# Kernel optimization log

Hardware: AMD Instinct MI355X
Metric: run time of the kernel (lower is better)

The kernel has to match this reference:

```python
import jax, jax.numpy as jnp
import numpy as np

N_NODES = 100000
N_EDGES = 1600000
D_FEAT = 64


def setup_inputs() -> dict:
    key = jax.random.key(0)
    k1, k2, k3, k4 = jax.random.split(key, 4)
    x = jax.random.normal(k1, (N_NODES, D_FEAT), dtype=jnp.float32)
    edge_values = jax.random.uniform(k2, (N_EDGES,), dtype=jnp.float32)
    # row-sorted targets mimic a coalesced sparse COO matrix
    target_index = jnp.sort(jax.random.randint(k3, (N_EDGES,), 0, N_NODES, dtype=jnp.int32))
    source_index = jax.random.randint(k4, (N_EDGES,), 0, N_NODES, dtype=jnp.int32)
    return {"x": x, "edge_values": edge_values,
            "target_index": target_index, "source_index": source_index}


def reference(x, edge_values, target_index, source_index):
    # sparsify_message: gather source rows -> [n_edges, d]
    msg = x[source_index]
    # scale by sparse neighborhood values
    msg = edge_values[:, None] * msg
    # aggregate: scatter-sum into target cells -> [n_nodes, d]
    out = jax.ops.segment_sum(msg, target_index, num_segments=N_NODES)
    return out
```

## Files before the change

### kernel.cpp

```cpp
#include <hip/hip_runtime.h>
#include <hip/hip_fp16.h>

#define N_NODES 100000
#define N_EDGES 1600000
#define D_FEAT 64

typedef __attribute__((ext_vector_type(4))) _Float16 half4v;

__global__ __launch_bounds__(256) void prep_kernel(
    const float4* __restrict__ x4,
    const int*    __restrict__ tgt,
    half4v*       __restrict__ xh,
    int*          __restrict__ row_ptr,
    int conv_blocks)
{
    const int bid = blockIdx.x;
    if (bid < conv_blocks) {
        int i = bid * 256 + threadIdx.x;
        if (i < N_NODES * 16) {
            float4 v = x4[i];
            half4v h;
            h.x = (_Float16)v.x; h.y = (_Float16)v.y;
            h.z = (_Float16)v.z; h.w = (_Float16)v.w;
            xh[i] = h;
        }
    } else {
        int e = (bid - conv_blocks) * 256 + threadIdx.x;
        if (e >= N_EDGES) return;
        int cur = tgt[e];
        int lo  = (e == 0) ? 0 : tgt[e - 1] + 1;
        for (int n = lo; n <= cur; ++n) row_ptr[n] = e;
        if (e == N_EDGES - 1) {
            for (int n = cur + 1; n <= N_NODES; ++n) row_ptr[n] = N_EDGES;
        }
    }
}

__global__ __launch_bounds__(256) void build_row_ptr(
    const int* __restrict__ tgt, int* __restrict__ row_ptr)
{
    int e = blockIdx.x * blockDim.x + threadIdx.x;
    if (e >= N_EDGES) return;
    int cur = tgt[e];
    int lo  = (e == 0) ? 0 : tgt[e - 1] + 1;
    for (int n = lo; n <= cur; ++n) row_ptr[n] = e;
    if (e == N_EDGES - 1) {
        for (int n = cur + 1; n <= N_NODES; ++n) row_ptr[n] = N_EDGES;
    }
}

#define GROUPS_PER_BLOCK 16
#define LDS_STRIDE_B     144

__global__ __launch_bounds__(256) void gather_sum_h(
    const half4v* __restrict__ xh,
    const float*  __restrict__ ev,
    const int*    __restrict__ src,
    const int*    __restrict__ row_ptr,
    float4*       __restrict__ out4)
{
    __shared__ char lds_raw[GROUPS_PER_BLOCK * LDS_STRIDE_B];

    const int tib  = threadIdx.x;
    const int gib  = tib >> 4;
    const int lane = tib & 15;
    const int node = blockIdx.x * GROUPS_PER_BLOCK + gib;
    if (node >= N_NODES) return;

    char* gbase = lds_raw + gib * LDS_STRIDE_B;

    const int start = row_ptr[node];
    const int end   = row_ptr[node + 1];

    float4 acc = make_float4(0.f, 0.f, 0.f, 0.f);

    for (int blk = start; blk < end; blk += 16) {
        const int bcnt = end - blk;

        int   s_ = 0; float w_ = 0.0f;
        if (lane < bcnt) { s_ = src[blk + lane]; w_ = ev[blk + lane]; }
        ((int2*)gbase)[lane] = make_int2(s_, __float_as_int(w_));

        const int nch = (min(bcnt, 16) + 3) >> 2;

        int4 m01 = ((const int4*)gbase)[0];
        int4 m23 = ((const int4*)gbase)[1];
        half4v x0 = xh[m01.x * 16 + lane];
        half4v x1 = xh[m01.z * 16 + lane];
        half4v x2 = xh[m23.x * 16 + lane];
        half4v x3 = xh[m23.z * 16 + lane];
        float w0 = __int_as_float(m01.y), w1 = __int_as_float(m01.w);
        float w2 = __int_as_float(m23.y), w3 = __int_as_float(m23.w);

        for (int c = 1; c < nch; ++c) {
            int4 n01 = ((const int4*)gbase)[2 * c];
            int4 n23 = ((const int4*)gbase)[2 * c + 1];
            half4v nx0 = xh[n01.x * 16 + lane];
            half4v nx1 = xh[n01.z * 16 + lane];
            half4v nx2 = xh[n23.x * 16 + lane];
            half4v nx3 = xh[n23.z * 16 + lane];

            acc.x = fmaf(w0, (float)x0.x, acc.x);
            acc.y = fmaf(w0, (float)x0.y, acc.y);
            acc.z = fmaf(w0, (float)x0.z, acc.z);
            acc.w = fmaf(w0, (float)x0.w, acc.w);
            acc.x = fmaf(w1, (float)x1.x, acc.x);
            acc.y = fmaf(w1, (float)x1.y, acc.y);
            acc.z = fmaf(w1, (float)x1.z, acc.z);
            acc.w = fmaf(w1, (float)x1.w, acc.w);
            acc.x = fmaf(w2, (float)x2.x, acc.x);
            acc.y = fmaf(w2, (float)x2.y, acc.y);
            acc.z = fmaf(w2, (float)x2.z, acc.z);
            acc.w = fmaf(w2, (float)x2.w, acc.w);
            acc.x = fmaf(w3, (float)x3.x, acc.x);
            acc.y = fmaf(w3, (float)x3.y, acc.y);
            acc.z = fmaf(w3, (float)x3.z, acc.z);
            acc.w = fmaf(w3, (float)x3.w, acc.w);

            x0 = nx0; x1 = nx1; x2 = nx2; x3 = nx3;
            w0 = __int_as_float(n01.y); w1 = __int_as_float(n01.w);
            w2 = __int_as_float(n23.y); w3 = __int_as_float(n23.w);
        }

        acc.x = fmaf(w0, (float)x0.x, acc.x);
        acc.y = fmaf(w0, (float)x0.y, acc.y);
        acc.z = fmaf(w0, (float)x0.z, acc.z);
        acc.w = fmaf(w0, (float)x0.w, acc.w);
        acc.x = fmaf(w1, (float)x1.x, acc.x);
        acc.y = fmaf(w1, (float)x1.y, acc.y);
        acc.z = fmaf(w1, (float)x1.z, acc.z);
        acc.w = fmaf(w1, (float)x1.w, acc.w);
        acc.x = fmaf(w2, (float)x2.x, acc.x);
        acc.y = fmaf(w2, (float)x2.y, acc.y);
        acc.z = fmaf(w2, (float)x2.z, acc.z);
        acc.w = fmaf(w2, (float)x2.w, acc.w);
        acc.x = fmaf(w3, (float)x3.x, acc.x);
        acc.y = fmaf(w3, (float)x3.y, acc.y);
        acc.z = fmaf(w3, (float)x3.z, acc.z);
        acc.w = fmaf(w3, (float)x3.w, acc.w);
    }

    out4[node * 16 + lane] = acc;
}

__global__ __launch_bounds__(256) void gather_sum_f32(
    const float4* __restrict__ x4,
    const float*  __restrict__ ev,
    const int*    __restrict__ src,
    const int*    __restrict__ row_ptr,
    float4*       __restrict__ out4)
{
    const int node = blockIdx.x * 4 + (threadIdx.x >> 6);
    if (node >= N_NODES) return;
    const int lane = threadIdx.x & 63;
    const int g    = lane >> 4;
    const int f    = lane & 15;

    const int start = row_ptr[node];
    const int end   = row_ptr[node + 1];

    float4 acc = make_float4(0.f, 0.f, 0.f, 0.f);
    if (start < end) {
        int  ea = start + g, eb = start + 4 + g;
        bool va = ea < end,  vb = eb < end;
        int  esa = va ? ea : start, esb = vb ? eb : start;
        float wa = va ? ev[esa] : 0.0f;
        float wb = vb ? ev[esb] : 0.0f;
        int   sa = src[esa];
        int   sb = src[esb];

        for (int e0 = start; e0 < end; e0 += 8) {
            const float4 xa = x4[sa * 16 + f];
            const float4 xb = x4[sb * 16 + f];
            const float cwa = wa, cwb = wb;
            {
                int  na = e0 + 8 + g, nb = e0 + 12 + g;
                bool vna = na < end,  vnb = nb < end;
                int  nsa = vna ? na : start, nsb = vnb ? nb : start;
                wa = vna ? ev[nsa] : 0.0f;
                wb = vnb ? ev[nsb] : 0.0f;
                sa = src[nsa];
                sb = src[nsb];
            }
            acc.x = fmaf(cwa, xa.x, acc.x);
            acc.y = fmaf(cwa, xa.y, acc.y);
            acc.z = fmaf(cwa, xa.z, acc.z);
            acc.w = fmaf(cwa, xa.w, acc.w);
            acc.x = fmaf(cwb, xb.x, acc.x);
            acc.y = fmaf(cwb, xb.y, acc.y);
            acc.z = fmaf(cwb, xb.z, acc.z);
            acc.w = fmaf(cwb, xb.w, acc.w);
        }
    }
    acc.x += __shfl_xor(acc.x, 16, 64);
    acc.y += __shfl_xor(acc.y, 16, 64);
    acc.z += __shfl_xor(acc.z, 16, 64);
    acc.w += __shfl_xor(acc.w, 16, 64);
    acc.x += __shfl_xor(acc.x, 32, 64);
    acc.y += __shfl_xor(acc.y, 32, 64);
    acc.z += __shfl_xor(acc.z, 32, 64);
    acc.w += __shfl_xor(acc.w, 32, 64);
    if (g == 0) out4[node * 16 + f] = acc;
}

extern "C" void kernel_launch(void* const* d_in, const int* in_sizes, int n_in,
                              void* d_out, int out_size, void* d_ws, size_t ws_size,
                              hipStream_t stream) {
    const float* x            = (const float*)d_in[0];
    const float* edge_values  = (const float*)d_in[1];
    const int*   target_index = (const int*)d_in[2];
    const int*   source_index = (const int*)d_in[3];
    float*       out          = (float*)d_out;

    const size_t rp_bytes = (size_t)(N_NODES + 1) * sizeof(int);
    const size_t xh_off   = (rp_bytes + 511) & ~(size_t)511;
    const size_t xh_bytes = (size_t)N_NODES * D_FEAT * sizeof(_Float16);
    const size_t need     = xh_off + xh_bytes;

    int* row_ptr = (int*)d_ws;

    if (ws_size >= need) {
        half4v* xh = (half4v*)((char*)d_ws + xh_off);
        const int conv_blocks = (N_NODES * 16 + 255) / 256;
        const int rp_blocks   = (N_EDGES + 255) / 256;
        prep_kernel<<<conv_blocks + rp_blocks, 256, 0, stream>>>(
            (const float4*)x, target_index, xh, row_ptr, conv_blocks);

        const int n_blocks = (N_NODES + GROUPS_PER_BLOCK - 1) / GROUPS_PER_BLOCK;
        gather_sum_h<<<n_blocks, 256, 0, stream>>>(
            xh, edge_values, source_index, row_ptr, (float4*)out);
    } else {
        build_row_ptr<<<(N_EDGES + 255) / 256, 256, 0, stream>>>(target_index, row_ptr);
        gather_sum_f32<<<(N_NODES + 3) / 4, 256, 0, stream>>>(
            (const float4*)x, edge_values, source_index, row_ptr, (float4*)out);
    }
}
```

Before: 120.1 us.

## Split fp16 feature table into four column slices for cache-local gather

The prep kernel now writes the fp16 copy of x in a sliced layout, with four 16-column slices each stored contiguously over all nodes. The gather kernel runs four times as many blocks, each handling one slice, so each slice's working set (about 3.2MB) is more likely to stay in cache during the random source gathers. Nontemporal loads and stores are added for streamed data. The cost is that each lane now loads only 2 bytes per gather and edge indices and weights are reread once per slice.

```diff
diff --git a/kernel.cpp b/kernel.cpp
--- a/kernel.cpp
+++ b/kernel.cpp
@@ -5,24 +5,31 @@
 #define N_EDGES 1600000
 #define D_FEAT 64
 
+#define SLICES 4
+
 typedef __attribute__((ext_vector_type(4))) _Float16 half4v;
+typedef __attribute__((ext_vector_type(4))) float    f32x4;
 
 __global__ __launch_bounds__(256) void prep_kernel(
-    const float4* __restrict__ x4,
-    const int*    __restrict__ tgt,
-    half4v*       __restrict__ xh,
-    int*          __restrict__ row_ptr,
+    const f32x4* __restrict__ x4,
+    const int*   __restrict__ tgt,
+    half4v*      __restrict__ xh4,
+    int*         __restrict__ row_ptr,
     int conv_blocks)
 {
     const int bid = blockIdx.x;
     if (bid < conv_blocks) {
         int i = bid * 256 + threadIdx.x;
         if (i < N_NODES * 16) {
-            float4 v = x4[i];
+            f32x4 v = __builtin_nontemporal_load(&x4[i]);
             half4v h;
             h.x = (_Float16)v.x; h.y = (_Float16)v.y;
             h.z = (_Float16)v.z; h.w = (_Float16)v.w;
-            xh[i] = h;
+            int n = i >> 4;
+            int g = i & 15;
+            int q = g >> 2;
+            int slot = g & 3;
+            __builtin_nontemporal_store(h, &xh4[(((q * N_NODES) + n) << 2) | slot]);
         }
     } else {
         int e = (bid - conv_blocks) * 256 + threadIdx.x;
@@ -52,95 +59,77 @@
 #define GROUPS_PER_BLOCK 16
 #define LDS_STRIDE_B     144
 
-__global__ __launch_bounds__(256) void gather_sum_h(
-    const half4v* __restrict__ xh,
-    const float*  __restrict__ ev,
-    const int*    __restrict__ src,
-    const int*    __restrict__ row_ptr,
-    float4*       __restrict__ out4)
+__global__ __launch_bounds__(256) void gather_sum_slice(
+    const _Float16* __restrict__ xh,
+    const float*    __restrict__ ev,
+    const int*      __restrict__ src,
+    const int*      __restrict__ row_ptr,
+    float*          __restrict__ out)
 {
     __shared__ char lds_raw[GROUPS_PER_BLOCK * LDS_STRIDE_B];
 
     const int tib  = threadIdx.x;
     const int gib  = tib >> 4;
     const int lane = tib & 15;
-    const int node = blockIdx.x * GROUPS_PER_BLOCK + gib;
+    const int q    = blockIdx.x & 3;
+    const int node = (blockIdx.x >> 2) * GROUPS_PER_BLOCK + gib;
     if (node >= N_NODES) return;
+
+    const _Float16* __restrict__ xq = xh + (size_t)q * (N_NODES * 16);
 
     char* gbase = lds_raw + gib * LDS_STRIDE_B;
 
     const int start = row_ptr[node];
     const int end   = row_ptr[node + 1];
 
-    float4 acc = make_float4(0.f, 0.f, 0.f, 0.f);
+    float acc = 0.0f;
 
     for (int blk = start; blk < end; blk += 16) {
         const int bcnt = end - blk;
 
         int   s_ = 0; float w_ = 0.0f;
-        if (lane < bcnt) { s_ = src[blk + lane]; w_ = ev[blk + lane]; }
+        if (lane < bcnt) {
+            s_ = __builtin_nontemporal_load(&src[blk + lane]);
+            w_ = __builtin_nontemporal_load(&ev[blk + lane]);
+        }
         ((int2*)gbase)[lane] = make_int2(s_, __float_as_int(w_));
 
         const int nch = (min(bcnt, 16) + 3) >> 2;
 
         int4 m01 = ((const int4*)gbase)[0];
         int4 m23 = ((const int4*)gbase)[1];
-        half4v x0 = xh[m01.x * 16 + lane];
-        half4v x1 = xh[m01.z * 16 + lane];
-        half4v x2 = xh[m23.x * 16 + lane];
-        half4v x3 = xh[m23.z * 16 + lane];
+        _Float16 x0 = xq[(m01.x << 4) + lane];
+        _Float16 x1 = xq[(m01.z << 4) + lane];
+        _Float16 x2 = xq[(m23.x << 4) + lane];
+        _Float16 x3 = xq[(m23.z << 4) + lane];
         float w0 = __int_as_float(m01.y), w1 = __int_as_float(m01.w);
         float w2 = __int_as_float(m23.y), w3 = __int_as_float(m23.w);
 
         for (int c = 1; c < nch; ++c) {
             int4 n01 = ((const int4*)gbase)[2 * c];
             int4 n23 = ((const int4*)gbase)[2 * c + 1];
-            half4v nx0 = xh[n01.x * 16 + lane];
-            half4v nx1 = xh[n01.z * 16 + lane];
-            half4v nx2 = xh[n23.x * 16 + lane];
-            half4v nx3 = xh[n23.z * 16 + lane];
-
-            acc.x = fmaf(w0, (float)x0.x, acc.x);
-            acc.y = fmaf(w0, (float)x0.y, acc.y);
-            acc.z = fmaf(w0, (float)x0.z, acc.z);
-            acc.w = fmaf(w0, (float)x0.w, acc.w);
-            acc.x = fmaf(w1, (float)x1.x, acc.x);
-            acc.y = fmaf(w1, (float)x1.y, acc.y);
-            acc.z = fmaf(w1, (float)x1.z, acc.z);
-            acc.w = fmaf(w1, (float)x1.w, acc.w);
-            acc.x = fmaf(w2, (float)x2.x, acc.x);
-            acc.y = fmaf(w2, (float)x2.y, acc.y);
-            acc.z = fmaf(w2, (float)x2.z, acc.z);
-            acc.w = fmaf(w2, (float)x2.w, acc.w);
-            acc.x = fmaf(w3, (float)x3.x, acc.x);
-            acc.y = fmaf(w3, (float)x3.y, acc.y);
-            acc.z = fmaf(w3, (float)x3.z, acc.z);
-            acc.w = fmaf(w3, (float)x3.w, acc.w);
+            _Float16 nx0 = xq[(n01.x << 4) + lane];
+            _Float16 nx1 = xq[(n01.z << 4) + lane];
+            _Float16 nx2 = xq[(n23.x << 4) + lane];
+            _Float16 nx3 = xq[(n23.z << 4) + lane];
+
+            acc = fmaf(w0, (float)x0, acc);
+            acc = fmaf(w1, (float)x1, acc);
+            acc = fmaf(w2, (float)x2, acc);
+            acc = fmaf(w3, (float)x3, acc);
 
             x0 = nx0; x1 = nx1; x2 = nx2; x3 = nx3;
             w0 = __int_as_float(n01.y); w1 = __int_as_float(n01.w);
             w2 = __int_as_float(n23.y); w3 = __int_as_float(n23.w);
         }
 
-        acc.x = fmaf(w0, (float)x0.x, acc.x);
-        acc.y = fmaf(w0, (float)x0.y, acc.y);
-        acc.z = fmaf(w0, (float)x0.z, acc.z);
-        acc.w = fmaf(w0, (float)x0.w, acc.w);
-        acc.x = fmaf(w1, (float)x1.x, acc.x);
-        acc.y = fmaf(w1, (float)x1.y, acc.y);
-        acc.z = fmaf(w1, (float)x1.z, acc.z);
-        acc.w = fmaf(w1, (float)x1.w, acc.w);
-        acc.x = fmaf(w2, (float)x2.x, acc.x);
-        acc.y = fmaf(w2, (float)x2.y, acc.y);
-        acc.z = fmaf(w2, (float)x2.z, acc.z);
-        acc.w = fmaf(w2, (float)x2.w, acc.w);
-        acc.x = fmaf(w3, (float)x3.x, acc.x);
-        acc.y = fmaf(w3, (float)x3.y, acc.y);
-        acc.z = fmaf(w3, (float)x3.z, acc.z);
-        acc.w = fmaf(w3, (float)x3.w, acc.w);
-    }
-
-    out4[node * 16 + lane] = acc;
+        acc = fmaf(w0, (float)x0, acc);
+        acc = fmaf(w1, (float)x1, acc);
+        acc = fmaf(w2, (float)x2, acc);
+        acc = fmaf(w3, (float)x3, acc);
+    }
+
+    __builtin_nontemporal_store(acc, &out[(size_t)node * 64 + (q << 4) + lane]);
 }
 
 __global__ __launch_bounds__(256) void gather_sum_f32(
@@ -220,15 +209,15 @@
     int* row_ptr = (int*)d_ws;
 
     if (ws_size >= need) {
-        half4v* xh = (half4v*)((char*)d_ws + xh_off);
+        _Float16* xh = (_Float16*)((char*)d_ws + xh_off);
         const int conv_blocks = (N_NODES * 16 + 255) / 256;
         const int rp_blocks   = (N_EDGES + 255) / 256;
         prep_kernel<<<conv_blocks + rp_blocks, 256, 0, stream>>>(
-            (const float4*)x, target_index, xh, row_ptr, conv_blocks);
-
-        const int n_blocks = (N_NODES + GROUPS_PER_BLOCK - 1) / GROUPS_PER_BLOCK;
-        gather_sum_h<<<n_blocks, 256, 0, stream>>>(
-            xh, edge_values, source_index, row_ptr, (float4*)out);
+            (const f32x4*)x, target_index, (half4v*)xh, row_ptr, conv_blocks);
+
+        const int n_blocks = SLICES * ((N_NODES + GROUPS_PER_BLOCK - 1) / GROUPS_PER_BLOCK);
+        gather_sum_slice<<<n_blocks, 256, 0, stream>>>(
+            xh, edge_values, source_index, row_ptr, out);
     } else {
         build_row_ptr<<<(N_EDGES + 255) / 256, 256, 0, stream>>>(target_index, row_ptr);
         gather_sum_f32<<<(N_NODES + 3) / 4, 256, 0, stream>>>(
```

After: 166.0 us. +38.3%, slower.
